# Kernel optimization log

Measured on AMD Instinct MI355X. Metric: run time of the kernel, lower is better.

Reference implementation:

```python
import jax, jax.numpy as jnp
import numpy as np

NEG_INF = -9e15  # matches torch's -9000000000000000.0 mask value


def setup_inputs() -> dict:
    key = jax.random.key(0)
    k1, k2, k3, k4 = jax.random.split(key, 4)
    B, F_in, T, N, F_out = 8, 64, 12, 512, 64
    inp = {
        "input": jax.random.normal(k1, (B, F_in, T, N), dtype=jnp.float32),
        "adj": jax.random.randint(k2, (B, T, N, N), 0, 2, dtype=jnp.int32),
        "W": jax.random.normal(k3, (F_in, F_out), dtype=jnp.float32),
        "a": jax.random.normal(k4, (2 * F_out, 1), dtype=jnp.float32),
    }
    return inp


def reference(input, adj, W, a):
    # input: [B, F_in, T, N], adj: [B, T, N, N]
    F_out = W.shape[1]
    x = jnp.transpose(input, (0, 2, 3, 1))          # [B, T, N, F_in]
    Wh = jnp.einsum('btnf,fo->btno', x, W)          # [B, T, N, F_out]
    # score decomposition: e[i,j] = leakyrelu(a1.Wh_i + a2.Wh_j)
    a1 = a[:F_out, 0]
    a2 = a[F_out:, 0]
    f1 = Wh @ a1                                    # [B, T, N]
    f2 = Wh @ a2                                    # [B, T, N]
    e = jax.nn.leaky_relu(f1[..., :, None] + f2[..., None, :], 0.2)
    e = jnp.where(adj > 0, e, NEG_INF)
    attn = jax.nn.softmax(e, axis=-1)               # [B, T, N, N]
    h = jnp.einsum('btij,btjo->btio', attn, Wh)     # [B, T, N, F_out]
    return jax.nn.elu(h)                            # concat=True -> elu
```

## Files before the change

kernel.cpp:

```cpp
#include <hip/hip_runtime.h>
#include <hip/hip_bf16.h>

typedef float fx4 __attribute__((ext_vector_type(4)));
typedef short i16x8 __attribute__((ext_vector_type(8)));
typedef unsigned short u16;

#define NEG_INF_F (-9.0e15f)

__device__ inline u16 f2bf(float v){
  __hip_bfloat16 h = __float2bfloat16(v);
  return *reinterpret_cast<u16*>(&h);
}

__global__ __launch_bounds__(256) void gat_prep(
    const float* __restrict__ input,
    const float* __restrict__ W,
    const float* __restrict__ Avec,
    u16*   __restrict__ whT,
    float* __restrict__ f1w,
    float* __restrict__ f2w)
{
  __shared__ float Wl[64*64];
  __shared__ float Al[128];
  const int tid = threadIdx.x;
  const int bt  = blockIdx.y;
  const int b   = bt / 12, t = bt % 12;
  const int n   = blockIdx.x * 256 + tid;

  {
    const fx4* src = (const fx4*)W;
    fx4* dst = (fx4*)Wl;
    #pragma unroll
    for (int i = 0; i < 4; ++i) dst[tid + 256*i] = src[tid + 256*i];
    if (tid < 32) ((fx4*)Al)[tid] = ((const fx4*)Avec)[tid];
  }
  __syncthreads();

  const float* xp = input + ((size_t)b*64*12 + t) * 512 + n;

  fx4 acc[16];
  #pragma unroll
  for (int i = 0; i < 16; ++i) acc[i] = (fx4){0.f,0.f,0.f,0.f};

  #pragma unroll 8
  for (int f = 0; f < 64; ++f) {
    float xv = xp[(size_t)f * 6144];
    const fx4* wr = (const fx4*)(Wl + f*64);
    #pragma unroll
    for (int o4 = 0; o4 < 16; ++o4) acc[o4] += xv * wr[o4];
  }

  float s1 = 0.f, s2 = 0.f;
  #pragma unroll
  for (int o4 = 0; o4 < 16; ++o4) {
    fx4 v  = acc[o4];
    fx4 w1 = ((const fx4*)Al)[o4];
    fx4 w2 = ((const fx4*)Al)[o4 + 16];
    s1 += v[0]*w1[0] + v[1]*w1[1] + v[2]*w1[2] + v[3]*w1[3];
    s2 += v[0]*w2[0] + v[1]*w2[1] + v[2]*w2[2] + v[3]*w2[3];
  }
  f1w[bt*512 + n] = s1;
  f2w[bt*512 + n] = s2;

  u16* wp = whT + (size_t)bt*64*512 + n;
  #pragma unroll
  for (int o4 = 0; o4 < 16; ++o4) {
    #pragma unroll
    for (int c = 0; c < 4; ++c)
      wp[(size_t)(o4*4 + c) * 512] = f2bf(acc[o4][c]);
  }
}

__global__ __launch_bounds__(256) void gat_attn(
    const int*   __restrict__ adj,
    const u16*   __restrict__ whT,
    const float* __restrict__ f1w,
    const float* __restrict__ f2w,
    float*       __restrict__ out)
{
  __shared__ float f2l[512];
  __shared__ float f1l[16];
  __shared__ float sums[16];
  __shared__ u16   attnl[16*512];

  const int tid = threadIdx.x;
  const int l   = tid & 63;
  const int w   = tid >> 6;
  const int bt  = blockIdx.y;
  const int it  = blockIdx.x;

  ((float2*)f2l)[tid] = ((const float2*)(f2w + bt*512))[tid];
  if (tid < 16) f1l[tid] = f1w[bt*512 + it*16 + tid];
  __syncthreads();

  const int R0     = w * 4;
  const int row_g0 = it*16 + R0;
  const int4* adj4 = (const int4*)(adj + (size_t)bt*512*512);

  int4 pre[4][2];
  #pragma unroll
  for (int p = 0; p < 4; ++p) {
    const int4* ar = adj4 + (size_t)(row_g0 + p) * 128;
    pre[p][0] = ar[l];
    pre[p][1] = ar[64 + l];
  }

  const fx4 f20 = ((const fx4*)f2l)[l];
  const fx4 f21 = ((const fx4*)f2l)[64 + l];

  float psum[4];
  #pragma unroll
  for (int r = 0; r < 4; ++r) {
    const int4 c0 = pre[r][0];
    const int4 c1 = pre[r][1];
    const float f1v = f1l[R0 + r];

    float e[8], m = NEG_INF_F;
#define GAT_E(idx, cc, ff) { float s = f1v + (ff); float lr = s > 0.f ? s : 0.2f*s; \
                             e[idx] = ((cc) > 0) ? lr : NEG_INF_F; m = fmaxf(m, e[idx]); }
    GAT_E(0, c0.x, f20[0]) GAT_E(1, c0.y, f20[1]) GAT_E(2, c0.z, f20[2]) GAT_E(3, c0.w, f20[3])
    GAT_E(4, c1.x, f21[0]) GAT_E(5, c1.y, f21[1]) GAT_E(6, c1.z, f21[2]) GAT_E(7, c1.w, f21[3])
#undef GAT_E
    #pragma unroll
    for (int off = 32; off >= 1; off >>= 1) m = fmaxf(m, __shfl_xor(m, off));

    float p[8], sum = 0.f;
    #pragma unroll
    for (int i = 0; i < 8; ++i) { p[i] = __expf(e[i] - m); sum += p[i]; }
    psum[r] = sum;

    const int rowR = R0 + r;
    const unsigned swz = (unsigned)((rowR & 7) << 4);
    char* base = (char*)attnl + rowR * 1024;
    ushort4 pk0, pk1;
    pk0.x = f2bf(p[0]); pk0.y = f2bf(p[1]); pk0.z = f2bf(p[2]); pk0.w = f2bf(p[3]);
    pk1.x = f2bf(p[4]); pk1.y = f2bf(p[5]); pk1.z = f2bf(p[6]); pk1.w = f2bf(p[7]);
    *(ushort4*)(base + (((unsigned)(      8*l)) ^ swz)) = pk0;
    *(ushort4*)(base + (((unsigned)(512 + 8*l)) ^ swz)) = pk1;
  }

  #pragma unroll
  for (int r = 0; r < 4; ++r) {
    #pragma unroll
    for (int off = 32; off >= 1; off >>= 1) psum[r] += __shfl_xor(psum[r], off);
  }
  if (l == 0) {
    #pragma unroll
    for (int r = 0; r < 4; ++r) sums[R0 + r] = psum[r];
  }

  __syncthreads();

  const int r = l & 15, q = l >> 4;
  const unsigned swzB = (unsigned)((r & 7) << 4);
  const char* aBase = (const char*)attnl + r * 1024;
  const u16*  wb    = whT + (size_t)bt*64*512 + (size_t)(w*16 + r)*512;
  fx4 acc = {0,0,0,0};

  #pragma unroll
  for (int jt = 0; jt < 512; jt += 32) {
    i16x8 af = *(const i16x8*)(aBase + (((unsigned)(jt*2 + q*16)) ^ swzB));
    i16x8 bf = *(const i16x8*)(wb + jt + 8*q);
    acc = __builtin_amdgcn_mfma_f32_16x16x32_bf16(af, bf, acc, 0, 0, 0);
  }

  float* op = out + ((size_t)bt*512 + it*16) * 64;
  #pragma unroll
  for (int rr = 0; rr < 4; ++rr) {
    const float rs = 1.0f / sums[q*4 + rr];
    float v = acc[rr] * rs;
    v = v > 0.f ? v : expm1f(v);
    op[(q*4 + rr)*64 + w*16 + r] = v;
  }
}

extern "C" void kernel_launch(void* const* d_in, const int* in_sizes, int n_in,
                              void* d_out, int out_size, void* d_ws, size_t ws_size,
                              hipStream_t stream) {
  const float* input = (const float*)d_in[0];
  const int*   adj   = (const int*)  d_in[1];
  const float* W     = (const float*)d_in[2];
  const float* Avec  = (const float*)d_in[3];
  float* out = (float*)d_out;

  char* ws = (char*)d_ws;
  u16*   whT = (u16*)ws;
  float* f1w = (float*)(ws + 6291456);
  float* f2w = (float*)(ws + 6291456 + 196608);

  gat_prep<<<dim3(2, 96), 256, 0, stream>>>(input, W, Avec, whT, f1w, f2w);
  gat_attn<<<dim3(32, 96), 256, 0, stream>>>(adj, whT, f1w, f2w, out);
}
```

Baseline: 62.29 us.

## Process 32 rows per attention block with bitmask adj and 2x2 MFMA tiling

Each attention block now handles 32 query rows instead of 16, halving the grid and the per-block f2 reloads. Each row is split across 16 lanes, so all 8 adjacency int4 loads per row are issued up front. The adjacency tile is packed into a 32-bit mask per lane, and the row max is computed from f2 alone, relying on leaky-relu being monotonic, which removes per-element score storage. The MFMA stage uses a 2x2 wave tiling where each wave computes two output column tiles, reusing the attention fragment. This trades fewer blocks for more registers and LDS per block, with a launch-bounds occupancy hint.

New measurement: 64.09 us. +2.9%, slower.

```diff
diff --git a/kernel.cpp b/kernel.cpp
--- a/kernel.cpp
+++ b/kernel.cpp
@@ -71,7 +71,7 @@
   }
 }
 
-__global__ __launch_bounds__(256) void gat_attn(
+__global__ __launch_bounds__(256, 4) void gat_attn(
     const int*   __restrict__ adj,
     const u16*   __restrict__ whT,
     const float* __restrict__ f1w,
@@ -79,98 +79,130 @@
     float*       __restrict__ out)
 {
   __shared__ float f2l[512];
-  __shared__ float f1l[16];
-  __shared__ float sums[16];
-  __shared__ u16   attnl[16*512];
+  __shared__ float f1l[32];
+  __shared__ float sums[32];
+  __shared__ u16   attnl[32*512];
 
   const int tid = threadIdx.x;
   const int l   = tid & 63;
   const int w   = tid >> 6;
+  const int pos = l & 15;
+  const int g   = l >> 4;
   const int bt  = blockIdx.y;
   const int it  = blockIdx.x;
 
   ((float2*)f2l)[tid] = ((const float2*)(f2w + bt*512))[tid];
-  if (tid < 16) f1l[tid] = f1w[bt*512 + it*16 + tid];
+  if (tid < 32) f1l[tid] = f1w[bt*512 + it*32 + tid];
   __syncthreads();
 
-  const int R0     = w * 4;
-  const int row_g0 = it*16 + R0;
-  const int4* adj4 = (const int4*)(adj + (size_t)bt*512*512);
-
-  int4 pre[4][2];
-  #pragma unroll
-  for (int p = 0; p < 4; ++p) {
-    const int4* ar = adj4 + (size_t)(row_g0 + p) * 128;
-    pre[p][0] = ar[l];
-    pre[p][1] = ar[64 + l];
-  }
-
-  const fx4 f20 = ((const fx4*)f2l)[l];
-  const fx4 f21 = ((const fx4*)f2l)[64 + l];
-
-  float psum[4];
-  #pragma unroll
-  for (int r = 0; r < 4; ++r) {
-    const int4 c0 = pre[r][0];
-    const int4 c1 = pre[r][1];
-    const float f1v = f1l[R0 + r];
-
-    float e[8], m = NEG_INF_F;
-#define GAT_E(idx, cc, ff) { float s = f1v + (ff); float lr = s > 0.f ? s : 0.2f*s; \
-                             e[idx] = ((cc) > 0) ? lr : NEG_INF_F; m = fmaxf(m, e[idx]); }
-    GAT_E(0, c0.x, f20[0]) GAT_E(1, c0.y, f20[1]) GAT_E(2, c0.z, f20[2]) GAT_E(3, c0.w, f20[3])
-    GAT_E(4, c1.x, f21[0]) GAT_E(5, c1.y, f21[1]) GAT_E(6, c1.z, f21[2]) GAT_E(7, c1.w, f21[3])
-#undef GAT_E
-    #pragma unroll
-    for (int off = 32; off >= 1; off >>= 1) m = fmaxf(m, __shfl_xor(m, off));
-
-    float p[8], sum = 0.f;
-    #pragma unroll
-    for (int i = 0; i < 8; ++i) { p[i] = __expf(e[i] - m); sum += p[i]; }
-    psum[r] = sum;
-
-    const int rowR = R0 + r;
-    const unsigned swz = (unsigned)((rowR & 7) << 4);
-    char* base = (char*)attnl + rowR * 1024;
-    ushort4 pk0, pk1;
-    pk0.x = f2bf(p[0]); pk0.y = f2bf(p[1]); pk0.z = f2bf(p[2]); pk0.w = f2bf(p[3]);
-    pk1.x = f2bf(p[4]); pk1.y = f2bf(p[5]); pk1.z = f2bf(p[6]); pk1.w = f2bf(p[7]);
-    *(ushort4*)(base + (((unsigned)(      8*l)) ^ swz)) = pk0;
-    *(ushort4*)(base + (((unsigned)(512 + 8*l)) ^ swz)) = pk1;
-  }
-
-  #pragma unroll
-  for (int r = 0; r < 4; ++r) {
-    #pragma unroll
-    for (int off = 32; off >= 1; off >>= 1) psum[r] += __shfl_xor(psum[r], off);
-  }
-  if (l == 0) {
-    #pragma unroll
-    for (int r = 0; r < 4; ++r) sums[R0 + r] = psum[r];
-  }
-
+  fx4 f2r[8];
+  #pragma unroll
+  for (int k = 0; k < 8; ++k) f2r[k] = ((const fx4*)f2l)[pos + 16*k];
+
+  const int4* adjp = (const int4*)(adj + (size_t)bt*512*512);
+  const int lr0 = w*8 + g;
+  const int lr1 = lr0 + 4;
+  const int4* rp0 = adjp + (size_t)(it*32 + lr0) * 128;
+  const int4* rp1 = adjp + (size_t)(it*32 + lr1) * 128;
+
+  int4 A0[8], A1[8];
+  #pragma unroll
+  for (int k = 0; k < 8; ++k) A0[k] = rp0[pos + 16*k];
+  #pragma unroll
+  for (int k = 0; k < 8; ++k) A1[k] = rp1[pos + 16*k];
+
+  unsigned m0 = 0u, m1 = 0u;
+  #pragma unroll
+  for (int k = 0; k < 8; ++k) {
+    if (A0[k].x > 0) m0 |= 1u << (4*k+0);
+    if (A0[k].y > 0) m0 |= 1u << (4*k+1);
+    if (A0[k].z > 0) m0 |= 1u << (4*k+2);
+    if (A0[k].w > 0) m0 |= 1u << (4*k+3);
+  }
+  #pragma unroll
+  for (int k = 0; k < 8; ++k) {
+    if (A1[k].x > 0) m1 |= 1u << (4*k+0);
+    if (A1[k].y > 0) m1 |= 1u << (4*k+1);
+    if (A1[k].z > 0) m1 |= 1u << (4*k+2);
+    if (A1[k].w > 0) m1 |= 1u << (4*k+3);
+  }
+
+  float ssum0 = 0.f, ssum1 = 0.f;
+  #pragma unroll
+  for (int p = 0; p < 2; ++p) {
+    const unsigned msk = p ? m1 : m0;
+    const int lrw = p ? lr1 : lr0;
+    const float f1v = f1l[lrw];
+
+    float mx = NEG_INF_F;
+    #pragma unroll
+    for (int k = 0; k < 8; ++k) {
+      #pragma unroll
+      for (int c = 0; c < 4; ++c)
+        mx = fmaxf(mx, ((msk >> (4*k+c)) & 1u) ? f2r[k][c] : NEG_INF_F);
+    }
+    mx = fmaxf(mx, __shfl_xor(mx, 1));
+    mx = fmaxf(mx, __shfl_xor(mx, 2));
+    mx = fmaxf(mx, __shfl_xor(mx, 4));
+    mx = fmaxf(mx, __shfl_xor(mx, 8));
+    const float tM = f1v + mx;
+    const float M  = fmaxf(tM, 0.2f*tM);
+
+    float sum = 0.f;
+    char* abase = (char*)attnl + lrw * 1024;
+    const unsigned swz = (unsigned)((lrw & 7) << 4);
+    #pragma unroll
+    for (int k = 0; k < 8; ++k) {
+      ushort4 pk;
+      float t, lrv, pv;
+      t = f1v + f2r[k][0]; lrv = fmaxf(t, 0.2f*t);
+      pv = ((msk>>(4*k+0))&1u) ? __expf(lrv - M) : 0.f; sum += pv; pk.x = f2bf(pv);
+      t = f1v + f2r[k][1]; lrv = fmaxf(t, 0.2f*t);
+      pv = ((msk>>(4*k+1))&1u) ? __expf(lrv - M) : 0.f; sum += pv; pk.y = f2bf(pv);
+      t = f1v + f2r[k][2]; lrv = fmaxf(t, 0.2f*t);
+      pv = ((msk>>(4*k+2))&1u) ? __expf(lrv - M) : 0.f; sum += pv; pk.z = f2bf(pv);
+      t = f1v + f2r[k][3]; lrv = fmaxf(t, 0.2f*t);
+      pv = ((msk>>(4*k+3))&1u) ? __expf(lrv - M) : 0.f; sum += pv; pk.w = f2bf(pv);
+      *(ushort4*)(abase + (((unsigned)(8*pos + 128*k)) ^ swz)) = pk;
+    }
+    if (p == 0) ssum0 = sum; else ssum1 = sum;
+  }
+
+  #pragma unroll
+  for (int off = 1; off <= 8; off <<= 1) {
+    ssum0 += __shfl_xor(ssum0, off);
+    ssum1 += __shfl_xor(ssum1, off);
+  }
+  if (pos == 0) { sums[lr0] = ssum0; sums[lr1] = ssum1; }
   __syncthreads();
 
-  const int r = l & 15, q = l >> 4;
+  const int q  = g;
+  const int r  = pos;
+  const int rt = w & 1;
+  const int ct = w >> 1;
   const unsigned swzB = (unsigned)((r & 7) << 4);
-  const char* aBase = (const char*)attnl + r * 1024;
-  const u16*  wb    = whT + (size_t)bt*64*512 + (size_t)(w*16 + r)*512;
-  fx4 acc = {0,0,0,0};
+  const char* aBase = (const char*)attnl + (rt*16 + r) * 1024;
+  const u16* wb0 = whT + (size_t)bt*64*512 + (size_t)(ct*16 + r)*512;
+  const u16* wb1 = wb0 + 32*512;
+  fx4 acc0 = {0,0,0,0}, acc1 = {0,0,0,0};
 
   #pragma unroll
   for (int jt = 0; jt < 512; jt += 32) {
     i16x8 af = *(const i16x8*)(aBase + (((unsigned)(jt*2 + q*16)) ^ swzB));
-    i16x8 bf = *(const i16x8*)(wb + jt + 8*q);
-    acc = __builtin_amdgcn_mfma_f32_16x16x32_bf16(af, bf, acc, 0, 0, 0);
-  }
-
-  float* op = out + ((size_t)bt*512 + it*16) * 64;
+    i16x8 b0 = *(const i16x8*)(wb0 + jt + 8*q);
+    i16x8 b1 = *(const i16x8*)(wb1 + jt + 8*q);
+    acc0 = __builtin_amdgcn_mfma_f32_16x16x32_bf16(af, b0, acc0, 0, 0, 0);
+    acc1 = __builtin_amdgcn_mfma_f32_16x16x32_bf16(af, b1, acc1, 0, 0, 0);
+  }
+
+  float* op = out + ((size_t)bt*512 + it*32 + rt*16) * 64;
   #pragma unroll
   for (int rr = 0; rr < 4; ++rr) {
-    const float rs = 1.0f / sums[q*4 + rr];
-    float v = acc[rr] * rs;
-    v = v > 0.f ? v : expm1f(v);
-    op[(q*4 + rr)*64 + w*16 + r] = v;
+    const float rs = 1.0f / sums[rt*16 + q*4 + rr];
+    float v0 = acc0[rr] * rs; v0 = v0 > 0.f ? v0 : expm1f(v0);
+    float v1 = acc1[rr] * rs; v1 = v1 > 0.f ? v1 : expm1f(v1);
+    op[(q*4 + rr)*64 + ct*16      + r] = v0;
+    op[(q*4 + rr)*64 + ct*16 + 32 + r] = v1;
   }
 }
 
@@ -189,5 +221,5 @@
   float* f2w = (float*)(ws + 6291456 + 196608);
 
   gat_prep<<<dim3(2, 96), 256, 0, stream>>>(input, W, Avec, whT, f1w, f2w);
-  gat_attn<<<dim3(32, 96), 256, 0, stream>>>(adj, whT, f1w, f2w, out);
-}
+  gat_attn<<<dim3(16, 96), 256, 0, stream>>>(adj, whT, f1w, f2w, out);
+}
```
